# Performance work log

Measured on AMD Instinct MI355X. Metric: run time of the kernel, lower is better.

## Reference

```python
import jax, jax.numpy as jnp
import numpy as np

VOCAB, TAGS, EDIM, HDIM = 50000, 32, 256, 512
HALF = HDIM // 2
NEG = -10000.0


def _lstm_dir(x, Wih, Whh, b, reverse):
    # x: [B,S,E]; Wih: [4H,E]; Whh: [4H,H]; b: [4H] (b_ih + b_hh fused).
    B = x.shape[0]
    H = Whh.shape[1]

    def cell(carry, xt):
        h, c = carry
        z = xt @ Wih.T + h @ Whh.T + b            # [B,4H], gate order i,f,g,o
        i, f, g, o = jnp.split(z, 4, axis=-1)
        c = jax.nn.sigmoid(f) * c + jax.nn.sigmoid(i) * jnp.tanh(g)
        h = jax.nn.sigmoid(o) * jnp.tanh(c)
        return (h, c), h

    h0 = jnp.zeros((B, H), x.dtype)
    xs = jnp.swapaxes(x, 0, 1)                    # [S,B,E]
    _, hs = jax.lax.scan(cell, (h0, h0), xs, reverse=reverse)
    return jnp.swapaxes(hs, 0, 1)                 # [B,S,H] aligned to input positions


def _viterbi(feats, trans):
    # feats: [B,S,T] emissions; trans[prev, next] as used in the original recursion.
    B, S, T = feats.shape
    v0 = jnp.full((B, T), NEG, feats.dtype).at[:, 0].set(0.0)

    def step(v, feat_t):
        scores = v[:, :, None] + trans[None]      # [B, prev, next]
        best = jnp.max(scores, axis=1)
        bp = jnp.argmax(scores, axis=1)           # [B,T]
        return best + feat_t, bp

    vT, bps = jax.lax.scan(step, v0, jnp.swapaxes(feats, 0, 1))   # bps: [S,B,T]
    term = vT + trans[0][None]                    # terminal uses transitions[0, :]
    best_scores = jnp.max(term, axis=1)           # [B]
    last_tag = jnp.argmax(term, axis=1)           # [B]

    bidx = jnp.arange(B)

    def back(tag, bp):
        return bp[bidx, tag], tag

    tag0, ys = jax.lax.scan(back, last_tag, bps[1:], reverse=True)  # ys[k] = tag at pos k+1
    paths = jnp.concatenate([tag0[:, None], jnp.swapaxes(ys, 0, 1)], axis=1)  # [B,S]
    return paths, best_scores


def setup_inputs() -> dict:
    key = jax.random.key(0)
    ks = jax.random.split(key, 12)
    B, S = 64, 256
    s = 0.05
    trans = jax.random.normal(ks[10], (TAGS, TAGS), jnp.float32)
    trans = trans.at[:, 0].set(NEG).at[0, :].set(NEG)
    return {
        "sentence": jax.random.randint(ks[0], (B, S), 0, VOCAB, jnp.int32),
        "embed": jax.random.normal(ks[1], (VOCAB, EDIM), jnp.float32) * s,
        "Wih_f": jax.random.normal(ks[2], (4 * HALF, EDIM), jnp.float32) * s,
        "Whh_f": jax.random.normal(ks[3], (4 * HALF, HALF), jnp.float32) * s,
        "b_f": jax.random.normal(ks[4], (4 * HALF,), jnp.float32) * s,
        "Wih_b": jax.random.normal(ks[5], (4 * HALF, EDIM), jnp.float32) * s,
        "Whh_b": jax.random.normal(ks[6], (4 * HALF, HALF), jnp.float32) * s,
        "b_b": jax.random.normal(ks[7], (4 * HALF,), jnp.float32) * s,
        "Wout": jax.random.normal(ks[8], (TAGS, HDIM), jnp.float32) * s,
        "bout": jax.random.normal(ks[9], (TAGS,), jnp.float32) * s,
        "trans": trans,
    }


def reference(sentence, embed, Wih_f, Whh_f, b_f, Wih_b, Whh_b, b_b, Wout, bout, trans):
    # Inference path: dropout is identity in eval mode.
    x = embed[sentence]                           # [B,S,E]
    h_f = _lstm_dir(x, Wih_f, Whh_f, b_f, reverse=False)
    h_b = _lstm_dir(x, Wih_b, Whh_b, b_b, reverse=True)
    h = jnp.concatenate([h_f, h_b], axis=-1)      # [B,S,HDIM]
    feats = h @ Wout.T + bout                     # [B,S,TAGS]
    paths, scores = _viterbi(feats, trans)
    return paths, scores
```

## Files before the change

### kernel.cpp

```cpp
#include <hip/hip_runtime.h>
#include <hip/hip_fp16.h>
#include <stdint.h>

typedef float  f32x4  __attribute__((ext_vector_type(4)));
typedef int    i32x4  __attribute__((ext_vector_type(4)));
typedef short  bf16x8 __attribute__((ext_vector_type(8)));
typedef _Float16 h2v  __attribute__((ext_vector_type(2)));

#define NEGV -10000.0f
#define LOG2E 1.442695041f

__device__ __forceinline__ unsigned short f32_to_bf16(float f){
  union { float f; uint32_t u; } v; v.f = f;
  uint32_t u = v.u;
  u += 0x7fffu + ((u >> 16) & 1u);
  return (unsigned short)(u >> 16);
}
__device__ __forceinline__ float bf16_lo(uint32_t u){
  union { uint32_t u; float f; } v; v.u = (u & 0xffffu) << 16; return v.f;
}
__device__ __forceinline__ float bf16_hi(uint32_t u){
  union { uint32_t u; float f; } v; v.u = u & 0xffff0000u; return v.f;
}
__device__ __forceinline__ float fsig(float x){
  return __builtin_amdgcn_rcpf(1.0f + __builtin_exp2f(-LOG2E * x));
}
__device__ __forceinline__ float ftanh_(float x){
  return 1.0f - 2.0f * __builtin_amdgcn_rcpf(1.0f + __builtin_exp2f(2.0f * LOG2E * x));
}
__device__ __forceinline__ uint32_t enc_i8(float x){
  int v = (int)rintf(x * 512.0f);
  v = v > 127 ? 127 : (v < -127 ? -127 : v);
  return (uint32_t)(v & 0xff);
}
__device__ __forceinline__ float fdot2f(uint32_t w, uint32_t h, float acc){
#if __has_builtin(__builtin_amdgcn_fdot2)
  union { uint32_t u; h2v h; } a, b;
  a.u = w; b.u = h;
  return __builtin_amdgcn_fdot2(a.h, b.h, acc, false);
#else
  acc += __half2float(__ushort_as_half((unsigned short)(w & 0xffffu))) *
         __half2float(__ushort_as_half((unsigned short)(h & 0xffffu)));
  acc += __half2float(__ushort_as_half((unsigned short)(w >> 16))) *
         __half2float(__ushort_as_half((unsigned short)(h >> 16)));
  return acc;
#endif
}
__device__ __forceinline__ void wg_barrier_lds(){
  __builtin_amdgcn_s_waitcnt(0xC07F);
  asm volatile("" ::: "memory");
  __builtin_amdgcn_s_barrier();
  asm volatile("" ::: "memory");
}
__device__ __forceinline__ void wave_lds_fence(){
  __builtin_amdgcn_s_waitcnt(0xC07F);
  asm volatile("" ::: "memory");
}

__global__ __launch_bounds__(256) void k_quant(
    const float* __restrict__ whh_f, const float* __restrict__ whh_b,
    uint32_t* __restrict__ wq)
{
  const int id  = blockIdx.x * 256 + threadIdx.x;
  const int dir = id >> 16;
  const int rem = id & 0xffff;
  const int np  = rem >> 6;
  const int d   = rem & 63;
  const int u = np >> 2, g = np & 3;
  const float* __restrict__ w = dir ? whh_b : whh_f;
  const float4 v = *(const float4*)(w + (size_t)(g * 256 + u) * 256 + d * 4);
  wq[id] = enc_i8(v.x) | (enc_i8(v.y) << 8) | (enc_i8(v.z) << 16) | (enc_i8(v.w) << 24);
}

__global__ __launch_bounds__(256) void k_xproj(
    const int* __restrict__ sent, const float* __restrict__ embed,
    const float* __restrict__ wih_f, const float* __restrict__ wih_b,
    const float* __restrict__ bias_f, const float* __restrict__ bias_b,
    unsigned short* __restrict__ xp)
{
  __shared__ __align__(16) short At[128 * 32];
  __shared__ __align__(16) short Bt[128 * 32];
  const int bid = blockIdx.x;
  const int tm = bid >> 4;
  const int tn = bid & 15;
  const int dir = tn >> 3;
  const int nloc0 = (tn & 7) * 128;
  const float* __restrict__ wsrc = dir ? wih_b : wih_f;
  const float* __restrict__ bsrc = dir ? bias_b : bias_f;

  const int tid = threadIdx.x;
  const int wv = tid >> 6;
  const int lane = tid & 63;
  const int lr = lane & 15;
  const int lq = lane >> 4;

  const int r  = tid >> 1;
  const int ch = (tid & 1) * 16;

  const int tok = sent[tm * 128 + r];
  const int nprow = nloc0 + r;
  const float* arow = embed + (size_t)tok * 256 + ch;
  const float* brow = wsrc + (size_t)((nprow & 3) * 256 + (nprow >> 2)) * 256 + ch;
  short* at_dst = At + r * 32 + ch;
  short* bt_dst = Bt + r * 32 + ch;

  f32x4 acc[2][8];
  #pragma unroll
  for (int i = 0; i < 2; i++)
    #pragma unroll
    for (int n = 0; n < 8; n++)
      acc[i][n] = (f32x4){0.f, 0.f, 0.f, 0.f};

  for (int k0 = 0; k0 < 256; k0 += 32) {
    #pragma unroll
    for (int qq = 0; qq < 4; qq++) {
      const float4 va = *(const float4*)(arow + k0 + qq * 4);
      const float4 vb = *(const float4*)(brow + k0 + qq * 4);
      short4 sa, sb;
      sa.x = (short)f32_to_bf16(va.x); sa.y = (short)f32_to_bf16(va.y);
      sa.z = (short)f32_to_bf16(va.z); sa.w = (short)f32_to_bf16(va.w);
      sb.x = (short)f32_to_bf16(vb.x); sb.y = (short)f32_to_bf16(vb.y);
      sb.z = (short)f32_to_bf16(vb.z); sb.w = (short)f32_to_bf16(vb.w);
      *(short4*)(at_dst + qq * 4) = sa;
      *(short4*)(bt_dst + qq * 4) = sb;
    }
    __syncthreads();
    bf16x8 bfr[8];
    #pragma unroll
    for (int n = 0; n < 8; n++)
      bfr[n] = *(const bf16x8*)(Bt + (n * 16 + lr) * 32 + lq * 8);
    #pragma unroll
    for (int i = 0; i < 2; i++) {
      const bf16x8 af = *(const bf16x8*)(At + (wv * 32 + i * 16 + lr) * 32 + lq * 8);
      #pragma unroll
      for (int n = 0; n < 8; n++)
        acc[i][n] = __builtin_amdgcn_mfma_f32_16x16x32_bf16(af, bfr[n], acc[i][n], 0, 0, 0);
    }
    __syncthreads();
  }
  #pragma unroll
  for (int i = 0; i < 2; i++) {
    #pragma unroll
    for (int n = 0; n < 8; n++) {
      const int nloc = nloc0 + n * 16 + lr;
      const float bias = bsrc[(nloc & 3) * 256 + (nloc >> 2)];
      #pragma unroll
      for (int rr = 0; rr < 4; rr++) {
        const int m = tm * 128 + wv * 32 + i * 16 + lq * 4 + rr;
        xp[(size_t)m * 2048 + dir * 1024 + nloc] = f32_to_bf16(acc[i][n][rr] + bias);
      }
    }
  }
}

__global__ __launch_bounds__(512, 2) void k_lstm(
    const unsigned short* __restrict__ xp, const uint32_t* __restrict__ wq,
    __half* __restrict__ hout)
{
  __shared__ __align__(16) unsigned char hbuf[2][256];
  const int bid = blockIdx.x;
  const int dir = bid & 1;
  const int b = bid >> 1;
  const int tid = threadIdx.x;
  const int w = tid >> 6;
  const int l = tid & 63;
  const int lr = l & 15;
  const int q = l >> 4;
  const int nio = lr & 7;
  const int u = w * 32 + nio * 4 + q;

  i32x4 afr[8][4];
  {
    const unsigned char* wb = (const unsigned char*)wq + (size_t)dir * 262144;
    #pragma unroll
    for (int ni = 0; ni < 8; ni++) {
      const unsigned char* rp = wb + (size_t)(w * 128 + ni * 16 + lr) * 256 + q * 16;
      #pragma unroll
      for (int kt = 0; kt < 4; kt++) {
        afr[ni][kt] = *(const i32x4*)(rp + kt * 64);
        asm volatile("" : "+v"(afr[ni][kt].x), "+v"(afr[ni][kt].y),
                          "+v"(afr[ni][kt].z), "+v"(afr[ni][kt].w));
      }
    }
  }
  if (tid < 64) ((uint32_t*)hbuf[0])[tid] = 0;
  float c = 0.0f;
  const unsigned short* xpb = xp + (size_t)b * (256 * 2048) + dir * 1024 + w * 128 + q * 4;
  __half* hb = hout + (size_t)b * (256 * 512) + dir * 256 + u;

  uint2 xa[8], xb[8];
  {
    const int t0 = dir ? 255 : 0;
    const int t1 = dir ? 254 : 1;
    #pragma unroll
    for (int ni = 0; ni < 8; ni++) {
      xa[ni] = *(const uint2*)(xpb + (size_t)t0 * 2048 + ni * 16);
      xb[ni] = *(const uint2*)(xpb + (size_t)t1 * 2048 + ni * 16);
    }
  }
  __syncthreads();

#define LSTM_STEP(SS, SRD, SWR, XC)                                          \
  {                                                                          \
    const int t_ = dir ? (255 - (SS)) : (SS);                                \
    i32x4 bfr[4];                                                            \
    _Pragma("unroll")                                                        \
    for (int kt = 0; kt < 4; kt++)                                           \
      bfr[kt] = *(const i32x4*)(&hbuf[SRD][kt * 64 + q * 16]);               \
    i32x4 acc[8];                                                            \
    _Pragma("unroll")                                                        \
    for (int ni = 0; ni < 8; ni++) acc[ni] = (i32x4){0, 0, 0, 0};            \
    _Pragma("unroll")                                                        \
    for (int kt = 0; kt < 4; kt++)                                           \
      _Pragma("unroll")                                                      \
      for (int ni = 0; ni < 8; ni++)                                         \
        acc[ni] = __builtin_amdgcn_mfma_i32_16x16x64_i8(                     \
            afr[ni][kt], bfr[kt], acc[ni], 0, 0, 0);                         \
    i32x4 zi = acc[0];                                                       \
    uint32_t x0 = XC[0].x, x1 = XC[0].y;                                     \
    _Pragma("unroll")                                                        \
    for (int ni = 1; ni < 8; ni++) {                                         \
      const bool own = (nio == ni);                                          \
      zi.x = own ? acc[ni].x : zi.x;                                         \
      zi.y = own ? acc[ni].y : zi.y;                                         \
      zi.z = own ? acc[ni].z : zi.z;                                         \
      zi.w = own ? acc[ni].w : zi.w;                                         \
      x0 = own ? XC[ni].x : x0;                                              \
      x1 = own ? XC[ni].y : x1;                                              \
    }                                                                        \
    const float SINV = 1.0f / 65536.0f;                                      \
    const float z_i = (float)zi.x * SINV + bf16_lo(x0);                      \
    const float z_f = (float)zi.y * SINV + bf16_hi(x0);                      \
    const float z_g = (float)zi.z * SINV + bf16_lo(x1);                      \
    const float z_o = (float)zi.w * SINV + bf16_hi(x1);                      \
    const float ig = fsig(z_i), fg = fsig(z_f);                              \
    const float gg = ftanh_(z_g), og = fsig(z_o);                            \
    c = fg * c + ig * gg;                                                    \
    const float h_ = og * ftanh_(c);                                         \
    {               \
      int spf = (SS) + 2; spf = spf > 255 ? 255 : spf;                       \
      const int tpf = dir ? (255 - spf) : spf;                               \
      const unsigned short* xr = xpb + (size_t)tpf * 2048;                   \
      _Pragma("unroll")                                                      \
      for (int ni = 0; ni < 8; ni++)                                         \
        XC[ni] = *(const uint2*)(xr + ni * 16);                              \
    }                                                                        \
    if (lr < 8) {                                                            \
      hb[(size_t)t_ * 512] = __float2half(h_);                               \
      int hq = (int)rintf(h_ * 128.0f);                                      \
      hq = hq > 127 ? 127 : (hq < -127 ? -127 : hq);                         \
      hbuf[SWR][u] = (unsigned char)(hq & 0xff);                             \
    }                                                                        \
    wg_barrier_lds();                                                        \
  }

  for (int s = 0; s < 256; s += 2) {
    LSTM_STEP(s,     0, 1, xa)
    LSTM_STEP(s + 1, 1, 0, xb)
  }
#undef LSTM_STEP
}

__global__ __launch_bounds__(256) void k_feats(
    const __half* __restrict__ hg, const float* __restrict__ wout,
    const float* __restrict__ bout, float* __restrict__ feats)
{
  __shared__ uint32_t W2[32 * 257];
  __shared__ float bo[32];
  const int b  = blockIdx.x >> 2;
  const int t0 = (blockIdx.x & 3) * 64;
  const int tid = threadIdx.x;
  #pragma unroll
  for (int i = 0; i < 32; i++) {
    const float2 v = *(const float2*)(wout + (size_t)i * 512 + tid * 2);
    const uint32_t lo = (uint32_t)__half_as_ushort(__float2half(v.x));
    const uint32_t hi = (uint32_t)__half_as_ushort(__float2half(v.y));
    W2[i * 257 + tid] = lo | (hi << 16);
  }
  if (tid < 32) bo[tid] = bout[tid];
  __syncthreads();
  const int n = tid & 31;
  const int tg = tid >> 5;
  const uint32_t* hrow0 = (const uint32_t*)(hg + (size_t)b * (256 * 512));
  for (int tt = 0; tt < 8; tt++) {
    const int t = t0 + tg * 8 + tt;
    const uint4* hr = (const uint4*)(hrow0 + t * 256);
    float a0 = 0.f, a1 = 0.f, a2 = 0.f, a3 = 0.f;
    #pragma unroll
    for (int qd = 0; qd < 64; qd++) {
      const uint4 hq = hr[qd];
      a0 = fdot2f(W2[n * 257 + qd * 4 + 0], hq.x, a0);
      a1 = fdot2f(W2[n * 257 + qd * 4 + 1], hq.y, a1);
      a2 = fdot2f(W2[n * 257 + qd * 4 + 2], hq.z, a2);
      a3 = fdot2f(W2[n * 257 + qd * 4 + 3], hq.w, a3);
    }
    feats[((size_t)b * 256 + t) * 32 + n] = bo[n] + ((a0 + a1) + (a2 + a3));
  }
}

__global__ __launch_bounds__(64) void k_viterbi(
    const float* __restrict__ feats, const float* __restrict__ trans,
    int* __restrict__ paths, float* __restrict__ scores)
{
  __shared__ float vbuf[2][2][32];
  __shared__ unsigned char bp[2][256][32];
  __shared__ int tags[2][256];
  const int tid = threadIdx.x;
  const int s = tid >> 5;
  const int n = tid & 31;
  const int b = blockIdx.x * 2 + s;
  float tcol[32];
  #pragma unroll
  for (int p = 0; p < 32; p++) tcol[p] = trans[p * 32 + n];
  float v = (n == 0) ? 0.0f : NEGV;
  const float* fb = feats + (size_t)b * (256 * 32) + n;
  float xf0 = fb[0], xf1 = fb[32], xf2 = fb[64], xf3 = fb[96];

  for (int t = 0; t < 256; t++) {
    const int ph = t & 1;
    vbuf[ph][s][n] = v;
    wave_lds_fence();
    float best = -3.0e38f; int bpi = 0;
    #pragma unroll
    for (int i = 0; i < 8; i++) {
      const float4 q4 = ((const float4*)vbuf[ph][s])[i];
      float sc;
      sc = q4.x + tcol[i * 4 + 0]; if (sc > best) { best = sc; bpi = i * 4 + 0; }
      sc = q4.y + tcol[i * 4 + 1]; if (sc > best) { best = sc; bpi = i * 4 + 1; }
      sc = q4.z + tcol[i * 4 + 2]; if (sc > best) { best = sc; bpi = i * 4 + 2; }
      sc = q4.w + tcol[i * 4 + 3]; if (sc > best) { best = sc; bpi = i * 4 + 3; }
    }
    bp[s][t][n] = (unsigned char)bpi;
    v = best + xf0;
    xf0 = xf1; xf1 = xf2; xf2 = xf3;
    {
      int tp = t + 4; tp = tp > 255 ? 255 : tp;
      xf3 = fb[(size_t)tp * 32];
    }
  }
  vbuf[0][s][n] = v + tcol[0];
  wave_lds_fence();
  if (n == 0) {
    float bs = vbuf[0][s][0]; int bt = 0;
    #pragma unroll 1
    for (int p = 1; p < 32; p++) {
      if (vbuf[0][s][p] > bs) { bs = vbuf[0][s][p]; bt = p; }
    }
    scores[b] = bs;
    int tg = bt;
    tags[s][255] = tg;
    #pragma unroll 1
    for (int t = 255; t >= 1; t--) {
      tg = bp[s][t][tg];
      tags[s][t - 1] = tg;
    }
  }
  wave_lds_fence();
  #pragma unroll
  for (int i = 0; i < 8; i++) {
    const int idx = i * 64 + tid;
    const int ss = idx >> 8;
    const int t = idx & 255;
    paths[(size_t)(blockIdx.x * 2 + ss) * 256 + t] = tags[ss][t];
  }
}

extern "C" void kernel_launch(void* const* d_in, const int* in_sizes, int n_in,
                              void* d_out, int out_size, void* d_ws, size_t ws_size,
                              hipStream_t stream)
{
  (void)in_sizes; (void)n_in; (void)out_size; (void)ws_size;
  const int*   sent  = (const int*)d_in[0];
  const float* embed = (const float*)d_in[1];
  const float* wih_f = (const float*)d_in[2];
  const float* whh_f = (const float*)d_in[3];
  const float* b_f   = (const float*)d_in[4];
  const float* wih_b = (const float*)d_in[5];
  const float* whh_b = (const float*)d_in[6];
  const float* b_b   = (const float*)d_in[7];
  const float* wout  = (const float*)d_in[8];
  const float* bout  = (const float*)d_in[9];
  const float* trans = (const float*)d_in[10];

  char* ws = (char*)d_ws;
  unsigned short* XP = (unsigned short*)(ws);
  __half*   Hg = (__half*)(ws + 67108864);
  uint32_t* WQ = (uint32_t*)(ws + 83886080);
  float*    FT = (float*)(ws + 84410368);

  int*   paths  = (int*)d_out;
  float* scores = (float*)d_out + 16384;

  k_quant  <<<dim3(512),  dim3(256), 0, stream>>>(whh_f, whh_b, WQ);
  k_xproj  <<<dim3(2048), dim3(256), 0, stream>>>(sent, embed, wih_f, wih_b, b_f, b_b, XP);
  k_lstm   <<<dim3(128),  dim3(512), 0, stream>>>(XP, WQ, Hg);
  k_feats  <<<dim3(256),  dim3(256), 0, stream>>>(Hg, wout, bout, FT);
  k_viterbi<<<dim3(32),   dim3(64),  0, stream>>>(FT, trans, paths, scores);
}
```

Before: 578.8 us.

## Pack argmax index into float mantissa in Viterbi and load only owned xproj slice

In the LSTM recurrence each lane now loads only the pre-projected input slice for the gate block it owns, instead of loading all eight slices and picking one with selects. This cuts global loads and register use per step. The Viterbi max-plus step packs the predecessor index into the low five mantissa bits of each score, so the argmax becomes a tree of fmaxf with no branches. All scores are offset by -20000 to keep them negative, so the integer-ordered packing stays consistent, and the offset is added back to the final score. This truncates the low mantissa bits of scores and can change tie-breaking and near-tie argmax choices compared with the reference.

```diff
diff --git a/kernel.cpp b/kernel.cpp
--- a/kernel.cpp
+++ b/kernel.cpp
@@ -56,6 +56,10 @@
   __builtin_amdgcn_s_waitcnt(0xC07F);
   asm volatile("" ::: "memory");
 }
+__device__ __forceinline__ float vpack(float sc, int p){
+  const int i = (__float_as_int(sc) & 0xFFFFFFE0) | p;
+  return __int_as_float(i);
+}
 
 __global__ __launch_bounds__(256) void k_quant(
     const float* __restrict__ whh_f, const float* __restrict__ whh_b,
@@ -185,18 +189,16 @@
   }
   if (tid < 64) ((uint32_t*)hbuf[0])[tid] = 0;
   float c = 0.0f;
-  const unsigned short* xpb = xp + (size_t)b * (256 * 2048) + dir * 1024 + w * 128 + q * 4;
+  const unsigned short* xpo = xp + (size_t)b * (256 * 2048) + dir * 1024
+                                 + w * 128 + nio * 16 + q * 4;
   __half* hb = hout + (size_t)b * (256 * 512) + dir * 256 + u;
 
-  uint2 xa[8], xb[8];
+  uint2 xa, xb;
   {
     const int t0 = dir ? 255 : 0;
     const int t1 = dir ? 254 : 1;
-    #pragma unroll
-    for (int ni = 0; ni < 8; ni++) {
-      xa[ni] = *(const uint2*)(xpb + (size_t)t0 * 2048 + ni * 16);
-      xb[ni] = *(const uint2*)(xpb + (size_t)t1 * 2048 + ni * 16);
-    }
+    xa = *(const uint2*)(xpo + (size_t)t0 * 2048);
+    xb = *(const uint2*)(xpo + (size_t)t1 * 2048);
   }
   __syncthreads();
 
@@ -217,7 +219,6 @@
         acc[ni] = __builtin_amdgcn_mfma_i32_16x16x64_i8(                     \
             afr[ni][kt], bfr[kt], acc[ni], 0, 0, 0);                         \
     i32x4 zi = acc[0];                                                       \
-    uint32_t x0 = XC[0].x, x1 = XC[0].y;                                     \
     _Pragma("unroll")                                                        \
     for (int ni = 1; ni < 8; ni++) {                                         \
       const bool own = (nio == ni);                                          \
@@ -225,25 +226,20 @@
       zi.y = own ? acc[ni].y : zi.y;                                         \
       zi.z = own ? acc[ni].z : zi.z;                                         \
       zi.w = own ? acc[ni].w : zi.w;                                         \
-      x0 = own ? XC[ni].x : x0;                                              \
-      x1 = own ? XC[ni].y : x1;                                              \
     }                                                                        \
     const float SINV = 1.0f / 65536.0f;                                      \
-    const float z_i = (float)zi.x * SINV + bf16_lo(x0);                      \
-    const float z_f = (float)zi.y * SINV + bf16_hi(x0);                      \
-    const float z_g = (float)zi.z * SINV + bf16_lo(x1);                      \
-    const float z_o = (float)zi.w * SINV + bf16_hi(x1);                      \
+    const float z_i = (float)zi.x * SINV + bf16_lo(XC.x);                    \
+    const float z_f = (float)zi.y * SINV + bf16_hi(XC.x);                    \
+    const float z_g = (float)zi.z * SINV + bf16_lo(XC.y);                    \
+    const float z_o = (float)zi.w * SINV + bf16_hi(XC.y);                    \
     const float ig = fsig(z_i), fg = fsig(z_f);                              \
     const float gg = ftanh_(z_g), og = fsig(z_o);                            \
     c = fg * c + ig * gg;                                                    \
     const float h_ = og * ftanh_(c);                                         \
-    {               \
+    {                                   \
       int spf = (SS) + 2; spf = spf > 255 ? 255 : spf;                       \
       const int tpf = dir ? (255 - spf) : spf;                               \
-      const unsigned short* xr = xpb + (size_t)tpf * 2048;                   \
-      _Pragma("unroll")                                                      \
-      for (int ni = 0; ni < 8; ni++)                                         \
-        XC[ni] = *(const uint2*)(xr + ni * 16);                              \
+      XC = *(const uint2*)(xpo + (size_t)tpf * 2048);                        \
     }                                                                        \
     if (lr < 8) {                                                            \
       hb[(size_t)t_ * 512] = __float2half(h_);                               \
@@ -312,7 +308,7 @@
   float tcol[32];
   #pragma unroll
   for (int p = 0; p < 32; p++) tcol[p] = trans[p * 32 + n];
-  float v = (n == 0) ? 0.0f : NEGV;
+  float v = (n == 0) ? -20000.0f : (NEGV - 20000.0f);
   const float* fb = feats + (size_t)b * (256 * 32) + n;
   float xf0 = fb[0], xf1 = fb[32], xf2 = fb[64], xf3 = fb[96];
 
@@ -320,17 +316,22 @@
     const int ph = t & 1;
     vbuf[ph][s][n] = v;
     wave_lds_fence();
-    float best = -3.0e38f; int bpi = 0;
-    #pragma unroll
-    for (int i = 0; i < 8; i++) {
-      const float4 q4 = ((const float4*)vbuf[ph][s])[i];
-      float sc;
-      sc = q4.x + tcol[i * 4 + 0]; if (sc > best) { best = sc; bpi = i * 4 + 0; }
-      sc = q4.y + tcol[i * 4 + 1]; if (sc > best) { best = sc; bpi = i * 4 + 1; }
-      sc = q4.z + tcol[i * 4 + 2]; if (sc > best) { best = sc; bpi = i * 4 + 2; }
-      sc = q4.w + tcol[i * 4 + 3]; if (sc > best) { best = sc; bpi = i * 4 + 3; }
-    }
-    bp[s][t][n] = (unsigned char)bpi;
+    float g0, g1, g2, g3, g4, g5, g6, g7;
+    #define VGROUP(GI, DST)                                                   \
+    {                                                                         \
+      const float4 q4 = ((const float4*)vbuf[ph][s])[GI];                     \
+      const float p0 = vpack(q4.x + tcol[GI * 4 + 0], GI * 4 + 0);            \
+      const float p1 = vpack(q4.y + tcol[GI * 4 + 1], GI * 4 + 1);            \
+      const float p2 = vpack(q4.z + tcol[GI * 4 + 2], GI * 4 + 2);            \
+      const float p3 = vpack(q4.w + tcol[GI * 4 + 3], GI * 4 + 3);            \
+      DST = fmaxf(fmaxf(p0, p1), fmaxf(p2, p3));                              \
+    }
+    VGROUP(0, g0) VGROUP(1, g1) VGROUP(2, g2) VGROUP(3, g3)
+    VGROUP(4, g4) VGROUP(5, g5) VGROUP(6, g6) VGROUP(7, g7)
+    #undef VGROUP
+    const float best = fmaxf(fmaxf(fmaxf(g0, g1), fmaxf(g2, g3)),
+                             fmaxf(fmaxf(g4, g5), fmaxf(g6, g7)));
+    bp[s][t][n] = (unsigned char)(__float_as_int(best) & 31);
     v = best + xf0;
     xf0 = xf1; xf1 = xf2; xf2 = xf3;
     {
@@ -346,7 +347,7 @@
     for (int p = 1; p < 32; p++) {
       if (vbuf[0][s][p] > bs) { bs = vbuf[0][s][p]; bt = p; }
     }
-    scores[b] = bs;
+    scores[b] = bs + 20000.0f;
     int tg = bt;
     tags[s][255] = tg;
     #pragma unroll 1
```

Result: faster. 541.9 us (-6.4%).
